# Performance work log

Hardware: AMD Instinct MI355X
Metric: run time of the kernel (lower is better)

## Reference

```python
import jax, jax.numpy as jnp
import numpy as np

D_MODEL = 1024
N_HEAD = 16
D_HEAD = D_MODEL // N_HEAD
BSZ, QLEN, MLEN = 2, 1024, 1024
KLEN = QLEN + MLEN


def setup_inputs() -> dict:
    key = jax.random.key(0)
    ks = jax.random.split(key, 10)
    s = 1.0 / np.sqrt(D_MODEL)
    inp = {
        "x": jax.random.normal(ks[0], (BSZ, QLEN, D_MODEL), jnp.float32),
        "mem": jax.random.normal(ks[1], (BSZ, MLEN, D_MODEL), jnp.float32),
        "pos_emb": jax.random.normal(ks[2], (KLEN, D_MODEL), jnp.float32),
        # causal mask with memory: query i may attend to key j iff j <= i + MLEN
        "attn_mask": (jnp.arange(KLEN)[None, :] > (jnp.arange(QLEN)[:, None] + MLEN))[None, None],
        "Wq": jax.random.normal(ks[3], (D_MODEL, D_MODEL), jnp.float32) * s,
        "Wk": jax.random.normal(ks[4], (D_MODEL, D_MODEL), jnp.float32) * s,
        "Wv": jax.random.normal(ks[5], (D_MODEL, D_MODEL), jnp.float32) * s,
        "Wr": jax.random.normal(ks[6], (D_MODEL, D_MODEL), jnp.float32) * s,
        "Wo": jax.random.normal(ks[7], (D_MODEL, D_MODEL), jnp.float32) * s,
        "r_w_bias": jax.random.normal(ks[8], (N_HEAD, D_HEAD), jnp.float32) * 0.02,
        "r_r_bias": jax.random.normal(ks[9], (N_HEAD, D_HEAD), jnp.float32) * 0.02,
    }
    return inp


def _rel_shift(x):
    # x: [b, n, q, k]
    b, n, q, k = x.shape
    x_padded = jnp.pad(x, ((0, 0), (0, 0), (0, 0), (1, 0)))  # zero column at front
    x_padded = x_padded.reshape(b, n, k + 1, q)
    return x_padded[:, :, 1:].reshape(b, n, q, k)


def reference(x, mem, pos_emb, attn_mask, Wq, Wk, Wv, Wr, Wo, r_w_bias, r_r_bias):
    bsz, qlen, _ = x.shape
    k_input = jnp.concatenate([mem, x], axis=1)
    klen = k_input.shape[1]
    scale = 1.0 / np.sqrt(D_HEAD)

    # projections -> [b, n, len, d]
    q = jnp.einsum('bqe,de->bqd', x, Wq).reshape(bsz, qlen, N_HEAD, D_HEAD).transpose(0, 2, 1, 3)
    k = jnp.einsum('bke,de->bkd', k_input, Wk).reshape(bsz, klen, N_HEAD, D_HEAD).transpose(0, 2, 1, 3)
    v = jnp.einsum('bke,de->bkd', k_input, Wv).reshape(bsz, klen, N_HEAD, D_HEAD).transpose(0, 2, 1, 3)
    r = jnp.einsum('ke,de->kd', pos_emb, Wr).reshape(klen, N_HEAD, D_HEAD).transpose(1, 0, 2)  # [n,k,d]

    AC = jnp.einsum('bnqd,bnkd->bnqk', q + r_w_bias[None, :, None, :], k)
    BD = jnp.einsum('bnqd,nkd->bnqk', q + r_r_bias[None, :, None, :], r)
    BD = _rel_shift(BD)

    attn_score = (AC + BD) * scale
    attn_score = jnp.where(attn_mask, -jnp.inf, attn_score)
    attn_prob = jax.nn.softmax(attn_score, axis=-1)

    attn_vec = jnp.einsum('bnqk,bnkd->bnqd', attn_prob, v)
    attn_vec = attn_vec.transpose(0, 2, 1, 3).reshape(bsz, qlen, N_HEAD * D_HEAD)
    return jnp.einsum('bqd,ed->bqe', attn_vec, Wo)
```

## Files before the change

kernel.cpp:

```cpp
#include <hip/hip_runtime.h>


#define B_SZ 2
#define QLEN 1024
#define MLEN 1024
#define KLEN 2048
#define DMODEL 1024
#define NH 16
#define DH 64

typedef _Float16 f16;
typedef __attribute__((ext_vector_type(8))) _Float16 f16x8;
typedef __attribute__((ext_vector_type(4))) _Float16 f16x4;
typedef __attribute__((ext_vector_type(4))) float f32x4;

__device__ __forceinline__ f16 f2h(float v) { return (f16)v; }
__device__ __forceinline__ float h2f(f16 v) { return (float)v; }

__device__ __forceinline__ f32x4 mfma16(f16x8 a, f16x8 b, f32x4 c) {
  return __builtin_amdgcn_mfma_f32_16x16x32_f16(a, b, c, 0, 0, 0);
}

__global__ __launch_bounds__(256) void convert_kernel(const float* __restrict__ src,
                                                      f16* __restrict__ dst, int n4) {
  const int i = blockIdx.x * 256 + threadIdx.x;
  if (i >= n4) return;
  const float4 v = reinterpret_cast<const float4*>(src)[i];
  f16x4 o = {(f16)v.x, (f16)v.y, (f16)v.z, (f16)v.w};
  reinterpret_cast<f16x4*>(dst)[i] = o;
}

__global__ __launch_bounds__(256) void pack_weights_kernel(
    const float* __restrict__ Wq, const float* __restrict__ Wk,
    const float* __restrict__ Wv, const float* __restrict__ Wr,
    const float* __restrict__ Wo, f16* __restrict__ Wqb, f16* __restrict__ Wkb,
    f16* __restrict__ Wvb, f16* __restrict__ Wrb, f16* __restrict__ Wob) {
  const float* src;
  f16* dst;
  switch (blockIdx.y) {
    case 0: src = Wq; dst = Wqb; break;
    case 1: src = Wk; dst = Wkb; break;
    case 2: src = Wv; dst = Wvb; break;
    case 3: src = Wr; dst = Wrb; break;
    default: src = Wo; dst = Wob; break;
  }
  const int i = blockIdx.x * 256 + threadIdx.x;
  const float4 v = reinterpret_cast<const float4*>(src)[i];
  f16x4 o = {(f16)v.x, (f16)v.y, (f16)v.z, (f16)v.w};
  reinterpret_cast<f16x4*>(dst)[i] = o;
}

__global__ __launch_bounds__(256) void build_kin_kernel(const float* __restrict__ x,
                                                        const float* __restrict__ mem,
                                                        f16* __restrict__ kin,
                                                        f16* __restrict__ xb) {
  const int i = blockIdx.x * 256 + threadIdx.x;
  const int per_b = KLEN * DMODEL / 4;
  const int b = i / per_b;
  const int rem = i - b * per_b;
  const int row = rem / (DMODEL / 4);
  const int cc = (rem - row * (DMODEL / 4)) * 4;
  const float* src = (row < MLEN)
      ? mem + ((size_t)b * MLEN + row) * DMODEL + cc
      : x + ((size_t)b * QLEN + (row - MLEN)) * DMODEL + cc;
  const float4 v = *reinterpret_cast<const float4*>(src);
  f16x4 o = {(f16)v.x, (f16)v.y, (f16)v.z, (f16)v.w};
  *reinterpret_cast<f16x4*>(kin + (size_t)i * 4) = o;
  if (row >= MLEN)
    *reinterpret_cast<f16x4*>(&xb[((size_t)b * QLEN + (row - MLEN)) * DMODEL + cc]) = o;
}

__global__ __launch_bounds__(256) void proj_kernel(
    const f16* __restrict__ Xb, const f16* __restrict__ Kin,
    const f16* __restrict__ Pos, const f16* __restrict__ Wqb,
    const f16* __restrict__ Wkb, const f16* __restrict__ Wvb,
    const f16* __restrict__ Wrb, f16* __restrict__ Qwb, f16* __restrict__ Qrb,
    f16* __restrict__ Kbb, f16* __restrict__ Vbb, f16* __restrict__ Rbb,
    const float* __restrict__ rwb, const float* __restrict__ rrb) {
  const int y = blockIdx.y;
  const f16 *A, *Bm;
  f16 *C0, *C1 = nullptr;
  int bm;
  bool dual = false;
  if (y < 16)      { A = Xb;  Bm = Wqb; C0 = Qwb; C1 = Qrb; bm = y * 128; dual = true; }
  else if (y < 48) { A = Kin; Bm = Wkb; C0 = Kbb; bm = (y - 16) * 128; }
  else if (y < 80) { A = Kin; Bm = Wvb; C0 = Vbb; bm = (y - 48) * 128; }
  else             { A = Pos; Bm = Wrb; C0 = Rbb; bm = (y - 80) * 128; }

  const int bn = blockIdx.x * 128;
  const int tid = threadIdx.x;
  const int wave = tid >> 6, lane = tid & 63;
  const int wr = wave >> 1, wc = wave & 1;
  const int lr = lane & 15, hi = lane >> 4;

  __shared__ f16 As[128][40];
  __shared__ f16 Bs[128][40];

  f32x4 acc[4][4];
#pragma unroll
  for (int m = 0; m < 4; ++m)
#pragma unroll
    for (int n = 0; n < 4; ++n) acc[m][n] = f32x4{0.f, 0.f, 0.f, 0.f};

  for (int k0 = 0; k0 < DMODEL; k0 += 32) {
#pragma unroll
    for (int it = 0; it < 2; ++it) {
      const int c = it * 256 + tid;
      const int row = c >> 2, col8 = (c & 3) << 3;
      *reinterpret_cast<f16x8*>(&As[row][col8]) =
          *reinterpret_cast<const f16x8*>(&A[(size_t)(bm + row) * DMODEL + k0 + col8]);
      *reinterpret_cast<f16x8*>(&Bs[row][col8]) =
          *reinterpret_cast<const f16x8*>(&Bm[(size_t)(bn + row) * DMODEL + k0 + col8]);
    }
    __syncthreads();
    f16x8 af[4], bf[4];
#pragma unroll
    for (int m = 0; m < 4; ++m)
      af[m] = *reinterpret_cast<const f16x8*>(&As[wr * 64 + m * 16 + lr][hi * 8]);
#pragma unroll
    for (int n = 0; n < 4; ++n)
      bf[n] = *reinterpret_cast<const f16x8*>(&Bs[wc * 64 + n * 16 + lr][hi * 8]);
#pragma unroll
    for (int m = 0; m < 4; ++m)
#pragma unroll
      for (int n = 0; n < 4; ++n) acc[m][n] = mfma16(af[m], bf[n], acc[m][n]);
    __syncthreads();
  }

#pragma unroll
  for (int m = 0; m < 4; ++m)
#pragma unroll
    for (int n = 0; n < 4; ++n)
#pragma unroll
      for (int r = 0; r < 4; ++r) {
        const int grow = bm + wr * 64 + m * 16 + hi * 4 + r;
        const int gcol = bn + wc * 64 + n * 16 + lr;
        const float v = acc[m][n][r];
        if (dual) {
          C0[(size_t)grow * DMODEL + gcol] = f2h(v + rwb[gcol]);
          C1[(size_t)grow * DMODEL + gcol] = f2h(v + rrb[gcol]);
        } else {
          C0[(size_t)grow * DMODEL + gcol] = f2h(v);
        }
      }
}

__global__ __launch_bounds__(256) void gemm_out_kernel(const f16* __restrict__ A,
                                                       const f16* __restrict__ Bm,
                                                       float* __restrict__ C) {
  const int bm = blockIdx.y * 128, bn = blockIdx.x * 128;
  const int tid = threadIdx.x;
  const int wave = tid >> 6, lane = tid & 63;
  const int wr = wave >> 1, wc = wave & 1;
  const int lr = lane & 15, hi = lane >> 4;

  __shared__ f16 As[128][40];
  __shared__ f16 Bs[128][40];

  f32x4 acc[4][4];
#pragma unroll
  for (int m = 0; m < 4; ++m)
#pragma unroll
    for (int n = 0; n < 4; ++n) acc[m][n] = f32x4{0.f, 0.f, 0.f, 0.f};

  for (int k0 = 0; k0 < DMODEL; k0 += 32) {
#pragma unroll
    for (int it = 0; it < 2; ++it) {
      const int c = it * 256 + tid;
      const int row = c >> 2, col8 = (c & 3) << 3;
      *reinterpret_cast<f16x8*>(&As[row][col8]) =
          *reinterpret_cast<const f16x8*>(&A[(size_t)(bm + row) * DMODEL + k0 + col8]);
      *reinterpret_cast<f16x8*>(&Bs[row][col8]) =
          *reinterpret_cast<const f16x8*>(&Bm[(size_t)(bn + row) * DMODEL + k0 + col8]);
    }
    __syncthreads();
    f16x8 af[4], bf[4];
#pragma unroll
    for (int m = 0; m < 4; ++m)
      af[m] = *reinterpret_cast<const f16x8*>(&As[wr * 64 + m * 16 + lr][hi * 8]);
#pragma unroll
    for (int n = 0; n < 4; ++n)
      bf[n] = *reinterpret_cast<const f16x8*>(&Bs[wc * 64 + n * 16 + lr][hi * 8]);
#pragma unroll
    for (int m = 0; m < 4; ++m)
#pragma unroll
      for (int n = 0; n < 4; ++n) acc[m][n] = mfma16(af[m], bf[n], acc[m][n]);
    __syncthreads();
  }

#pragma unroll
  for (int m = 0; m < 4; ++m)
#pragma unroll
    for (int n = 0; n < 4; ++n)
#pragma unroll
      for (int r = 0; r < 4; ++r)
        C[(size_t)(bm + wr * 64 + m * 16 + hi * 4 + r) * DMODEL + bn + wc * 64 +
          n * 16 + lr] = acc[m][n][r];
}

__global__ __launch_bounds__(512) void attn_kernel(
    const f16* __restrict__ Qw, const f16* __restrict__ Qr,
    const f16* __restrict__ Kb, const f16* __restrict__ Vb,
    const f16* __restrict__ Rb, f16* __restrict__ AV) {
  const int qb = blockIdx.x * 128;
  const int n = blockIdx.y;
  const int b = blockIdx.z;
  const int tid = threadIdx.x;
  const int wave = tid >> 6, lane = tid & 63;
  const int lr = lane & 15, hi = lane >> 4;
  const int w0 = qb + wave * 16;

  __shared__ f16 Ks[64][72];
  __shared__ f16 Vs[64][72];
  __shared__ f16 PB[8][16][72];

  f16x8 qw[2], qr[2];
  {
    const size_t qbase = ((size_t)(b * QLEN + w0 + lr)) * DMODEL + n * DH;
#pragma unroll
    for (int kk = 0; kk < 2; ++kk) {
      qw[kk] = *reinterpret_cast<const f16x8*>(&Qw[qbase + kk * 32 + hi * 8]);
      qr[kk] = *reinterpret_cast<const f16x8*>(&Qr[qbase + kk * 32 + hi * 8]);
    }
  }

  f32x4 o[4];
#pragma unroll
  for (int df = 0; df < 4; ++df) o[df] = f32x4{0.f, 0.f, 0.f, 0.f};
  float mrow[4], lrow[4];
#pragma unroll
  for (int r = 0; r < 4; ++r) { mrow[r] = -1e30f; lrow[r] = 0.f; }

  const f16* Rn = Rb + n * DH;
  const int jtiles = (qb + 128 + MLEN) >> 6;

  for (int jt = 0; jt < jtiles; ++jt) {
    const int j0 = jt << 6;
    const size_t kvbase = ((size_t)(b * KLEN + j0)) * DMODEL + n * DH;
    {
      const int c = tid;
      const int krow = c >> 3, kcol8 = (c & 7) << 3;
      *reinterpret_cast<f16x8*>(&Ks[krow][kcol8]) =
          *reinterpret_cast<const f16x8*>(&Kb[kvbase + (size_t)krow * DMODEL + kcol8]);
      const int vrow = c & 63, vcol8 = ((c >> 6) & 7) << 3;
      const f16x8 vv =
          *reinterpret_cast<const f16x8*>(&Vb[kvbase + (size_t)vrow * DMODEL + vcol8]);
#pragma unroll
      for (int e = 0; e < 8; ++e) Vs[vcol8 + e][vrow] = vv[e];
    }
    __syncthreads();

    f32x4 s[4];
#pragma unroll
    for (int nf = 0; nf < 4; ++nf) s[nf] = f32x4{0.f, 0.f, 0.f, 0.f};
#pragma unroll
    for (int kk = 0; kk < 2; ++kk)
#pragma unroll
      for (int nf = 0; nf < 4; ++nf) {
        const f16x8 kf =
            *reinterpret_cast<const f16x8*>(&Ks[nf * 16 + lr][kk * 32 + hi * 8]);
        s[nf] = mfma16(qw[kk], kf, s[nf]);
      }

    const int u0 = j0 + QLEN - 16 - w0;
    f32x4 bd[5];
#pragma unroll
    for (int nt = 0; nt < 5; ++nt) bd[nt] = f32x4{0.f, 0.f, 0.f, 0.f};
#pragma unroll
    for (int nt = 0; nt < 5; ++nt) {
      const int u = u0 + nt * 16 + lr;
      const int uc = u < KLEN ? u : KLEN - 1;
#pragma unroll
      for (int kk = 0; kk < 2; ++kk) {
        const f16x8 rf = *reinterpret_cast<const f16x8*>(
            &Rn[(size_t)uc * DMODEL + kk * 32 + hi * 8]);
        bd[nt] = mfma16(qr[kk], rf, bd[nt]);
      }
    }

    const int t0 = hi * 4;
#pragma unroll
    for (int nt = 0; nt < 5; ++nt)
#pragma unroll
      for (int r = 0; r < 4; ++r) {
        const int jl = nt * 16 + lr - 15 + t0 + r;
        if (jl >= 0 && jl < 64) PB[wave][t0 + r][jl] = f2h(bd[nt][r]);
      }
    __syncthreads();

    float sv[4][4];
#pragma unroll
    for (int r = 0; r < 4; ++r) {
      const int i = w0 + t0 + r;
#pragma unroll
      for (int nf = 0; nf < 4; ++nf) {
        const int j = j0 + nf * 16 + lr;
        sv[nf][r] = (j <= i + MLEN)
                        ? (s[nf][r] + h2f(PB[wave][t0 + r][nf * 16 + lr])) * 0.125f
                        : -1e30f;
      }
    }

#pragma unroll
    for (int r = 0; r < 4; ++r) {
      float tmax = fmaxf(fmaxf(sv[0][r], sv[1][r]), fmaxf(sv[2][r], sv[3][r]));
#pragma unroll
      for (int d = 1; d < 16; d <<= 1) tmax = fmaxf(tmax, __shfl_xor(tmax, d, 64));
      const float mnew = fmaxf(mrow[r], tmax);
      const float alpha = __expf(mrow[r] - mnew);
      mrow[r] = mnew;
      float tsum = 0.f;
#pragma unroll
      for (int nf = 0; nf < 4; ++nf) {
        const float p = __expf(sv[nf][r] - mnew);
        sv[nf][r] = p;
        tsum += p;
      }
#pragma unroll
      for (int d = 1; d < 16; d <<= 1) tsum += __shfl_xor(tsum, d, 64);
      lrow[r] = lrow[r] * alpha + tsum;
#pragma unroll
      for (int df = 0; df < 4; ++df) o[df][r] *= alpha;
    }

#pragma unroll
    for (int nf = 0; nf < 4; ++nf)
#pragma unroll
      for (int r = 0; r < 4; ++r) PB[wave][t0 + r][nf * 16 + lr] = f2h(sv[nf][r]);

#pragma unroll
    for (int kk = 0; kk < 2; ++kk) {
      const f16x8 pa =
          *reinterpret_cast<const f16x8*>(&PB[wave][lr][kk * 32 + hi * 8]);
#pragma unroll
      for (int df = 0; df < 4; ++df) {
        const f16x8 vb =
            *reinterpret_cast<const f16x8*>(&Vs[df * 16 + lr][kk * 32 + hi * 8]);
        o[df] = mfma16(pa, vb, o[df]);
      }
    }
    __syncthreads();
  }

#pragma unroll
  for (int df = 0; df < 4; ++df)
#pragma unroll
    for (int r = 0; r < 4; ++r) {
      const int i = w0 + hi * 4 + r;
      AV[((size_t)(b * QLEN + i)) * DMODEL + n * DH + df * 16 + lr] =
          f2h(o[df][r] / lrow[r]);
    }
}

extern "C" void kernel_launch(void* const* d_in, const int* in_sizes, int n_in,
                              void* d_out, int out_size, void* d_ws, size_t ws_size,
                              hipStream_t stream) {
  (void)in_sizes; (void)n_in; (void)out_size; (void)ws_size;
  const float* x   = (const float*)d_in[0];
  const float* mem = (const float*)d_in[1];
  const float* pos = (const float*)d_in[2];
  const float* Wq  = (const float*)d_in[4];
  const float* Wk  = (const float*)d_in[5];
  const float* Wv  = (const float*)d_in[6];
  const float* Wr  = (const float*)d_in[7];
  const float* Wo  = (const float*)d_in[8];
  const float* rwb = (const float*)d_in[9];
  const float* rrb = (const float*)d_in[10];
  float* out = (float*)d_out;

  char* ws = (char*)d_ws;
  size_t off = 0;
  auto alloc = [&](size_t elems) {
    void* p = (void*)(ws + off);
    off += (elems * sizeof(f16) + 255) & ~(size_t)255;
    return (f16*)p;
  };
  f16* Xb  = alloc((size_t)B_SZ * QLEN * DMODEL);
  f16* Kin = alloc((size_t)B_SZ * KLEN * DMODEL);
  f16* Pos = alloc((size_t)KLEN * DMODEL);
  f16* Wqb = alloc((size_t)DMODEL * DMODEL);
  f16* Wkb = alloc((size_t)DMODEL * DMODEL);
  f16* Wvb = alloc((size_t)DMODEL * DMODEL);
  f16* Wrb = alloc((size_t)DMODEL * DMODEL);
  f16* Wob = alloc((size_t)DMODEL * DMODEL);
  f16* Qwb = alloc((size_t)B_SZ * QLEN * DMODEL);
  f16* Qrb = alloc((size_t)B_SZ * QLEN * DMODEL);
  f16* Kbb = alloc((size_t)B_SZ * KLEN * DMODEL);
  f16* Vbb = alloc((size_t)B_SZ * KLEN * DMODEL);
  f16* Rbb = alloc((size_t)KLEN * DMODEL);
  f16* AVb = alloc((size_t)B_SZ * QLEN * DMODEL);

  pack_weights_kernel<<<dim3(1024, 5), dim3(256), 0, stream>>>(
      Wq, Wk, Wv, Wr, Wo, Wqb, Wkb, Wvb, Wrb, Wob);
  convert_kernel<<<dim3(KLEN * DMODEL / 4 / 256), dim3(256), 0, stream>>>(
      pos, Pos, KLEN * DMODEL / 4);
  build_kin_kernel<<<dim3(B_SZ * KLEN * DMODEL / 4 / 256), dim3(256), 0, stream>>>(
      x, mem, Kin, Xb);

  proj_kernel<<<dim3(8, 96), dim3(256), 0, stream>>>(
      Xb, Kin, Pos, Wqb, Wkb, Wvb, Wrb, Qwb, Qrb, Kbb, Vbb, Rbb, rwb, rrb);

  attn_kernel<<<dim3(QLEN / 128, NH, B_SZ), dim3(512), 0, stream>>>(
      Qwb, Qrb, Kbb, Vbb, Rbb, AVb);

  gemm_out_kernel<<<dim3(DMODEL / 128, B_SZ * QLEN / 128), dim3(256), 0, stream>>>(
      AVb, Wob, out);
}
```

Measured before the change: 350.1 us.

## Split attention over keys, prefetch K/V, shuffle rel-shift, direct-to-LDS GEMM loads

The GEMMs now share one core that loads 64-wide K slices straight into an XOR-swizzled LDS layout with global_load_lds, halving the barrier count per K step and avoiding bank conflicts. Attention splits each query block's key range into two halves, doubling the grid, and adds a combine kernel that merges the partial outputs using the saved row max and sum. Attention also prefetches the next K/V tile into registers while computing the current one. The relative shift is done with ds_bpermute lane shuffles instead of a round trip through LDS. The costs are an extra fp32 partial-output buffer, one more kernel launch, and higher register pressure.

After: 281.2 us. 1.25x faster.

```diff
diff --git a/kernel.cpp b/kernel.cpp
--- a/kernel.cpp
+++ b/kernel.cpp
@@ -19,6 +19,17 @@
 
 __device__ __forceinline__ f32x4 mfma16(f16x8 a, f16x8 b, f32x4 c) {
   return __builtin_amdgcn_mfma_f32_16x16x32_f16(a, b, c, 0, 0, 0);
+}
+
+__device__ __forceinline__ void gload_lds16(const f16* g, f16* l) {
+  __builtin_amdgcn_global_load_lds(
+      (const __attribute__((address_space(1))) void*)g,
+      (__attribute__((address_space(3))) void*)l, 16, 0, 0);
+}
+
+__device__ __forceinline__ float bperm(int srclane, float v) {
+  return __int_as_float(
+      __builtin_amdgcn_ds_bpermute(srclane << 2, __float_as_int(v)));
 }
 
 __global__ __launch_bounds__(256) void convert_kernel(const float* __restrict__ src,
@@ -70,6 +81,83 @@
     *reinterpret_cast<f16x4*>(&xb[((size_t)b * QLEN + (row - MLEN)) * DMODEL + cc]) = o;
 }
 
+template <int DUAL, int OUT_F32>
+__device__ __forceinline__ void gemm_core(const f16* __restrict__ A,
+                                          const f16* __restrict__ Bm,
+                                          void* __restrict__ C0v,
+                                          void* __restrict__ C1v,
+                                          const float* __restrict__ bias0,
+                                          const float* __restrict__ bias1, int bm,
+                                          int bn) {
+  const int tid = threadIdx.x;
+  const int wave = tid >> 6, lane = tid & 63;
+  const int wr = wave >> 1, wc = wave & 1;
+  const int lr = lane & 15, hi = lane >> 4;
+
+  __shared__ f16 As[128 * 64];
+  __shared__ f16 Bs[128 * 64];
+
+  f32x4 acc[4][4];
+#pragma unroll
+  for (int m = 0; m < 4; ++m)
+#pragma unroll
+    for (int n = 0; n < 4; ++n) acc[m][n] = f32x4{0.f, 0.f, 0.f, 0.f};
+
+  for (int k0 = 0; k0 < DMODEL; k0 += 64) {
+    __syncthreads();
+#pragma unroll
+    for (int it = 0; it < 4; ++it) {
+      const int c = it * 256 + tid;
+      const int row = c >> 3, c16 = c & 7;
+      const int c16s = c16 ^ (row & 7);
+      gload_lds16(&A[(size_t)(bm + row) * DMODEL + k0 + c16s * 8], &As[c * 8]);
+      gload_lds16(&Bm[(size_t)(bn + row) * DMODEL + k0 + c16s * 8], &Bs[c * 8]);
+    }
+    __syncthreads();
+#pragma unroll
+    for (int kk = 0; kk < 2; ++kk) {
+      f16x8 af[4], bf[4];
+#pragma unroll
+      for (int m = 0; m < 4; ++m) {
+        const int row = wr * 64 + m * 16 + lr;
+        const int colf = (kk * 32 + hi * 8) ^ ((row & 7) << 3);
+        af[m] = *reinterpret_cast<const f16x8*>(&As[row * 64 + colf]);
+      }
+#pragma unroll
+      for (int n = 0; n < 4; ++n) {
+        const int row = wc * 64 + n * 16 + lr;
+        const int colf = (kk * 32 + hi * 8) ^ ((row & 7) << 3);
+        bf[n] = *reinterpret_cast<const f16x8*>(&Bs[row * 64 + colf]);
+      }
+#pragma unroll
+      for (int m = 0; m < 4; ++m)
+#pragma unroll
+        for (int n = 0; n < 4; ++n) acc[m][n] = mfma16(af[m], bf[n], acc[m][n]);
+    }
+  }
+
+#pragma unroll
+  for (int m = 0; m < 4; ++m)
+#pragma unroll
+    for (int n = 0; n < 4; ++n)
+#pragma unroll
+      for (int r = 0; r < 4; ++r) {
+        const int grow = bm + wr * 64 + m * 16 + hi * 4 + r;
+        const int gcol = bn + wc * 64 + n * 16 + lr;
+        const float v = acc[m][n][r];
+        if constexpr (OUT_F32) {
+          reinterpret_cast<float*>(C0v)[(size_t)grow * DMODEL + gcol] = v;
+        } else if constexpr (DUAL) {
+          reinterpret_cast<f16*>(C0v)[(size_t)grow * DMODEL + gcol] =
+              f2h(v + bias0[gcol]);
+          reinterpret_cast<f16*>(C1v)[(size_t)grow * DMODEL + gcol] =
+              f2h(v + bias1[gcol]);
+        } else {
+          reinterpret_cast<f16*>(C0v)[(size_t)grow * DMODEL + gcol] = f2h(v);
+        }
+      }
+}
+
 __global__ __launch_bounds__(256) void proj_kernel(
     const f16* __restrict__ Xb, const f16* __restrict__ Kin,
     const f16* __restrict__ Pos, const f16* __restrict__ Wqb,
@@ -78,141 +166,47 @@
     f16* __restrict__ Kbb, f16* __restrict__ Vbb, f16* __restrict__ Rbb,
     const float* __restrict__ rwb, const float* __restrict__ rrb) {
   const int y = blockIdx.y;
-  const f16 *A, *Bm;
-  f16 *C0, *C1 = nullptr;
-  int bm;
-  bool dual = false;
-  if (y < 16)      { A = Xb;  Bm = Wqb; C0 = Qwb; C1 = Qrb; bm = y * 128; dual = true; }
-  else if (y < 48) { A = Kin; Bm = Wkb; C0 = Kbb; bm = (y - 16) * 128; }
-  else if (y < 80) { A = Kin; Bm = Wvb; C0 = Vbb; bm = (y - 48) * 128; }
-  else             { A = Pos; Bm = Wrb; C0 = Rbb; bm = (y - 80) * 128; }
-
   const int bn = blockIdx.x * 128;
-  const int tid = threadIdx.x;
-  const int wave = tid >> 6, lane = tid & 63;
-  const int wr = wave >> 1, wc = wave & 1;
-  const int lr = lane & 15, hi = lane >> 4;
-
-  __shared__ f16 As[128][40];
-  __shared__ f16 Bs[128][40];
-
-  f32x4 acc[4][4];
-#pragma unroll
-  for (int m = 0; m < 4; ++m)
-#pragma unroll
-    for (int n = 0; n < 4; ++n) acc[m][n] = f32x4{0.f, 0.f, 0.f, 0.f};
-
-  for (int k0 = 0; k0 < DMODEL; k0 += 32) {
-#pragma unroll
-    for (int it = 0; it < 2; ++it) {
-      const int c = it * 256 + tid;
-      const int row = c >> 2, col8 = (c & 3) << 3;
-      *reinterpret_cast<f16x8*>(&As[row][col8]) =
-          *reinterpret_cast<const f16x8*>(&A[(size_t)(bm + row) * DMODEL + k0 + col8]);
-      *reinterpret_cast<f16x8*>(&Bs[row][col8]) =
-          *reinterpret_cast<const f16x8*>(&Bm[(size_t)(bn + row) * DMODEL + k0 + col8]);
-    }
-    __syncthreads();
-    f16x8 af[4], bf[4];
-#pragma unroll
-    for (int m = 0; m < 4; ++m)
-      af[m] = *reinterpret_cast<const f16x8*>(&As[wr * 64 + m * 16 + lr][hi * 8]);
-#pragma unroll
-    for (int n = 0; n < 4; ++n)
-      bf[n] = *reinterpret_cast<const f16x8*>(&Bs[wc * 64 + n * 16 + lr][hi * 8]);
-#pragma unroll
-    for (int m = 0; m < 4; ++m)
-#pragma unroll
-      for (int n = 0; n < 4; ++n) acc[m][n] = mfma16(af[m], bf[n], acc[m][n]);
-    __syncthreads();
-  }
-
-#pragma unroll
-  for (int m = 0; m < 4; ++m)
-#pragma unroll
-    for (int n = 0; n < 4; ++n)
-#pragma unroll
-      for (int r = 0; r < 4; ++r) {
-        const int grow = bm + wr * 64 + m * 16 + hi * 4 + r;
-        const int gcol = bn + wc * 64 + n * 16 + lr;
-        const float v = acc[m][n][r];
-        if (dual) {
-          C0[(size_t)grow * DMODEL + gcol] = f2h(v + rwb[gcol]);
-          C1[(size_t)grow * DMODEL + gcol] = f2h(v + rrb[gcol]);
-        } else {
-          C0[(size_t)grow * DMODEL + gcol] = f2h(v);
-        }
-      }
+  if (y < 16) {
+    gemm_core<1, 0>(Xb, Wqb, Qwb, Qrb, rwb, rrb, y * 128, bn);
+  } else if (y < 48) {
+    gemm_core<0, 0>(Kin, Wkb, Kbb, nullptr, nullptr, nullptr, (y - 16) * 128, bn);
+  } else if (y < 80) {
+    gemm_core<0, 0>(Kin, Wvb, Vbb, nullptr, nullptr, nullptr, (y - 48) * 128, bn);
+  } else {
+    gemm_core<0, 0>(Pos, Wrb, Rbb, nullptr, nullptr, nullptr, (y - 80) * 128, bn);
+  }
 }
 
 __global__ __launch_bounds__(256) void gemm_out_kernel(const f16* __restrict__ A,
                                                        const f16* __restrict__ Bm,
                                                        float* __restrict__ C) {
-  const int bm = blockIdx.y * 128, bn = blockIdx.x * 128;
-  const int tid = threadIdx.x;
-  const int wave = tid >> 6, lane = tid & 63;
-  const int wr = wave >> 1, wc = wave & 1;
-  const int lr = lane & 15, hi = lane >> 4;
-
-  __shared__ f16 As[128][40];
-  __shared__ f16 Bs[128][40];
-
-  f32x4 acc[4][4];
-#pragma unroll
-  for (int m = 0; m < 4; ++m)
-#pragma unroll
-    for (int n = 0; n < 4; ++n) acc[m][n] = f32x4{0.f, 0.f, 0.f, 0.f};
-
-  for (int k0 = 0; k0 < DMODEL; k0 += 32) {
-#pragma unroll
-    for (int it = 0; it < 2; ++it) {
-      const int c = it * 256 + tid;
-      const int row = c >> 2, col8 = (c & 3) << 3;
-      *reinterpret_cast<f16x8*>(&As[row][col8]) =
-          *reinterpret_cast<const f16x8*>(&A[(size_t)(bm + row) * DMODEL + k0 + col8]);
-      *reinterpret_cast<f16x8*>(&Bs[row][col8]) =
-          *reinterpret_cast<const f16x8*>(&Bm[(size_t)(bn + row) * DMODEL + k0 + col8]);
-    }
-    __syncthreads();
-    f16x8 af[4], bf[4];
-#pragma unroll
-    for (int m = 0; m < 4; ++m)
-      af[m] = *reinterpret_cast<const f16x8*>(&As[wr * 64 + m * 16 + lr][hi * 8]);
-#pragma unroll
-    for (int n = 0; n < 4; ++n)
-      bf[n] = *reinterpret_cast<const f16x8*>(&Bs[wc * 64 + n * 16 + lr][hi * 8]);
-#pragma unroll
-    for (int m = 0; m < 4; ++m)
-#pragma unroll
-      for (int n = 0; n < 4; ++n) acc[m][n] = mfma16(af[m], bf[n], acc[m][n]);
-    __syncthreads();
-  }
-
-#pragma unroll
-  for (int m = 0; m < 4; ++m)
-#pragma unroll
-    for (int n = 0; n < 4; ++n)
-#pragma unroll
-      for (int r = 0; r < 4; ++r)
-        C[(size_t)(bm + wr * 64 + m * 16 + hi * 4 + r) * DMODEL + bn + wc * 64 +
-          n * 16 + lr] = acc[m][n][r];
+  gemm_core<0, 1>(A, Bm, C, nullptr, nullptr, nullptr, blockIdx.y * 128,
+                  blockIdx.x * 128);
 }
 
 __global__ __launch_bounds__(512) void attn_kernel(
     const f16* __restrict__ Qw, const f16* __restrict__ Qr,
     const f16* __restrict__ Kb, const f16* __restrict__ Vb,
-    const f16* __restrict__ Rb, f16* __restrict__ AV) {
-  const int qb = blockIdx.x * 128;
+    const f16* __restrict__ Rb, float* __restrict__ Opart,
+    float2* __restrict__ MLp) {
+  const int qi = blockIdx.x >> 1, half = blockIdx.x & 1;
+  const int qb = qi * 128;
   const int n = blockIdx.y;
   const int b = blockIdx.z;
   const int tid = threadIdx.x;
   const int wave = tid >> 6, lane = tid & 63;
   const int lr = lane & 15, hi = lane >> 4;
+  const int t0 = hi * 4;
   const int w0 = qb + wave * 16;
+
+  const int T = (qb + 128 + MLEN) >> 6;
+  const int jt_beg = half ? (T >> 1) : 0;
+  const int jt_end = half ? T : (T >> 1);
 
   __shared__ f16 Ks[64][72];
   __shared__ f16 Vs[64][72];
-  __shared__ f16 PB[8][16][72];
+  __shared__ f16 Ps[8][16][72];
 
   f16x8 qw[2], qr[2];
   {
@@ -232,23 +226,30 @@
   for (int r = 0; r < 4; ++r) { mrow[r] = -1e30f; lrow[r] = 0.f; }
 
   const f16* Rn = Rb + n * DH;
-  const int jtiles = (qb + 128 + MLEN) >> 6;
-
-  for (int jt = 0; jt < jtiles; ++jt) {
+
+  const int krow = tid >> 3, kc8 = (tid & 7) << 3;
+  const int vrow = tid & 63, vc8 = ((tid >> 6) & 7) << 3;
+  f16x8 kreg, vreg;
+  auto issue = [&](int jt) {
+    const size_t kvb = ((size_t)(b * KLEN + (jt << 6))) * DMODEL + n * DH;
+    kreg = *reinterpret_cast<const f16x8*>(&Kb[kvb + (size_t)krow * DMODEL + kc8]);
+    vreg = *reinterpret_cast<const f16x8*>(&Vb[kvb + (size_t)vrow * DMODEL + vc8]);
+  };
+  auto commit = [&]() {
+    *reinterpret_cast<f16x8*>(&Ks[krow][kc8]) = kreg;
+#pragma unroll
+    for (int e = 0; e < 8; ++e) Vs[vc8 + e][vrow] = vreg[e];
+  };
+
+  issue(jt_beg);
+  commit();
+  __syncthreads();
+
+  for (int jt = jt_beg; jt < jt_end; ++jt) {
+    const bool hn = (jt + 1 < jt_end);
+    if (hn) issue(jt + 1);
+
     const int j0 = jt << 6;
-    const size_t kvbase = ((size_t)(b * KLEN + j0)) * DMODEL + n * DH;
-    {
-      const int c = tid;
-      const int krow = c >> 3, kcol8 = (c & 7) << 3;
-      *reinterpret_cast<f16x8*>(&Ks[krow][kcol8]) =
-          *reinterpret_cast<const f16x8*>(&Kb[kvbase + (size_t)krow * DMODEL + kcol8]);
-      const int vrow = c & 63, vcol8 = ((c >> 6) & 7) << 3;
-      const f16x8 vv =
-          *reinterpret_cast<const f16x8*>(&Vb[kvbase + (size_t)vrow * DMODEL + vcol8]);
-#pragma unroll
-      for (int e = 0; e < 8; ++e) Vs[vcol8 + e][vrow] = vv[e];
-    }
-    __syncthreads();
 
     f32x4 s[4];
 #pragma unroll
@@ -278,32 +279,26 @@
       }
     }
 
-    const int t0 = hi * 4;
-#pragma unroll
-    for (int nt = 0; nt < 5; ++nt)
-#pragma unroll
-      for (int r = 0; r < 4; ++r) {
-        const int jl = nt * 16 + lr - 15 + t0 + r;
-        if (jl >= 0 && jl < 64) PB[wave][t0 + r][jl] = f2h(bd[nt][r]);
-      }
-    __syncthreads();
-
-    float sv[4][4];
 #pragma unroll
     for (int r = 0; r < 4; ++r) {
+      const int off = 15 - t0 - r;
+      const int sl = lr + off;
+      const int srclane = hi * 16 + (sl & 15);
+      const bool cross = sl >= 16;
       const int i = w0 + t0 + r;
 #pragma unroll
       for (int nf = 0; nf < 4; ++nf) {
+        const float x0 = bperm(srclane, bd[nf][r]);
+        const float x1 = bperm(srclane, bd[nf + 1][r]);
+        const float bv = cross ? x1 : x0;
         const int j = j0 + nf * 16 + lr;
-        sv[nf][r] = (j <= i + MLEN)
-                        ? (s[nf][r] + h2f(PB[wave][t0 + r][nf * 16 + lr])) * 0.125f
-                        : -1e30f;
+        s[nf][r] = (j <= i + MLEN) ? (s[nf][r] + bv) * 0.125f : -1e30f;
       }
     }
 
 #pragma unroll
     for (int r = 0; r < 4; ++r) {
-      float tmax = fmaxf(fmaxf(sv[0][r], sv[1][r]), fmaxf(sv[2][r], sv[3][r]));
+      float tmax = fmaxf(fmaxf(s[0][r], s[1][r]), fmaxf(s[2][r], s[3][r]));
 #pragma unroll
       for (int d = 1; d < 16; d <<= 1) tmax = fmaxf(tmax, __shfl_xor(tmax, d, 64));
       const float mnew = fmaxf(mrow[r], tmax);
@@ -312,8 +307,8 @@
       float tsum = 0.f;
 #pragma unroll
       for (int nf = 0; nf < 4; ++nf) {
-        const float p = __expf(sv[nf][r] - mnew);
-        sv[nf][r] = p;
+        const float p = __expf(s[nf][r] - mnew);
+        s[nf][r] = p;
         tsum += p;
       }
 #pragma unroll
@@ -326,12 +321,12 @@
 #pragma unroll
     for (int nf = 0; nf < 4; ++nf)
 #pragma unroll
-      for (int r = 0; r < 4; ++r) PB[wave][t0 + r][nf * 16 + lr] = f2h(sv[nf][r]);
+      for (int r = 0; r < 4; ++r) Ps[wave][t0 + r][nf * 16 + lr] = f2h(s[nf][r]);
 
 #pragma unroll
     for (int kk = 0; kk < 2; ++kk) {
       const f16x8 pa =
-          *reinterpret_cast<const f16x8*>(&PB[wave][lr][kk * 32 + hi * 8]);
+          *reinterpret_cast<const f16x8*>(&Ps[wave][lr][kk * 32 + hi * 8]);
 #pragma unroll
       for (int df = 0; df < 4; ++df) {
         const f16x8 vb =
@@ -339,17 +334,49 @@
         o[df] = mfma16(pa, vb, o[df]);
       }
     }
+
     __syncthreads();
-  }
-
+    if (hn) commit();
+    __syncthreads();
+  }
+
+  const size_t obase =
+      (((size_t)(half * B_SZ + b) * NH + n) * QLEN + w0 + t0) * DH;
 #pragma unroll
   for (int df = 0; df < 4; ++df)
 #pragma unroll
-    for (int r = 0; r < 4; ++r) {
-      const int i = w0 + hi * 4 + r;
-      AV[((size_t)(b * QLEN + i)) * DMODEL + n * DH + df * 16 + lr] =
-          f2h(o[df][r] / lrow[r]);
-    }
+    for (int r = 0; r < 4; ++r)
+      Opart[obase + (size_t)r * DH + df * 16 + lr] = o[df][r];
+  if (lr == 0) {
+    const size_t mbase = ((size_t)(half * B_SZ + b) * NH + n) * QLEN + w0 + t0;
+#pragma unroll
+    for (int r = 0; r < 4; ++r) MLp[mbase + r] = float2{mrow[r], lrow[r]};
+  }
+}
+
+__global__ __launch_bounds__(256) void combine_kernel(const float* __restrict__ Op,
+                                                      const float2* __restrict__ ML,
+                                                      f16* __restrict__ AV) {
+  const int idx = blockIdx.x * 256 + threadIdx.x;
+  const int d4 = idx & 15;
+  const int i = (idx >> 4) & 1023;
+  const int n = (idx >> 14) & 15;
+  const int b = idx >> 18;
+  const size_t r0 = ((size_t)(b * NH + n)) * QLEN + i;
+  const size_t r1 = ((size_t)((B_SZ + b) * NH + n)) * QLEN + i;
+  const float2 ml0 = ML[r0], ml1 = ML[r1];
+  const float M = fmaxf(ml0.x, ml1.x);
+  const float e0 = __expf(ml0.x - M), e1 = __expf(ml1.x - M);
+  const float inv = 1.f / (ml0.y * e0 + ml1.y * e1);
+  const float4 o0 = *reinterpret_cast<const float4*>(&Op[r0 * DH + d4 * 4]);
+  const float4 o1 = *reinterpret_cast<const float4*>(&Op[r1 * DH + d4 * 4]);
+  f16x4 out;
+  out[0] = f2h((o0.x * e0 + o1.x * e1) * inv);
+  out[1] = f2h((o0.y * e0 + o1.y * e1) * inv);
+  out[2] = f2h((o0.z * e0 + o1.z * e1) * inv);
+  out[3] = f2h((o0.w * e0 + o1.w * e1) * inv);
+  *reinterpret_cast<f16x4*>(&AV[((size_t)(b * QLEN + i)) * DMODEL + n * DH + d4 * 4]) =
+      out;
 }
 
 extern "C" void kernel_launch(void* const* d_in, const int* in_sizes, int n_in,
@@ -370,25 +397,27 @@
 
   char* ws = (char*)d_ws;
   size_t off = 0;
-  auto alloc = [&](size_t elems) {
+  auto alloc = [&](size_t bytes) {
     void* p = (void*)(ws + off);
-    off += (elems * sizeof(f16) + 255) & ~(size_t)255;
-    return (f16*)p;
+    off += (bytes + 255) & ~(size_t)255;
+    return p;
   };
-  f16* Xb  = alloc((size_t)B_SZ * QLEN * DMODEL);
-  f16* Kin = alloc((size_t)B_SZ * KLEN * DMODEL);
-  f16* Pos = alloc((size_t)KLEN * DMODEL);
-  f16* Wqb = alloc((size_t)DMODEL * DMODEL);
-  f16* Wkb = alloc((size_t)DMODEL * DMODEL);
-  f16* Wvb = alloc((size_t)DMODEL * DMODEL);
-  f16* Wrb = alloc((size_t)DMODEL * DMODEL);
-  f16* Wob = alloc((size_t)DMODEL * DMODEL);
-  f16* Qwb = alloc((size_t)B_SZ * QLEN * DMODEL);
-  f16* Qrb = alloc((size_t)B_SZ * QLEN * DMODEL);
-  f16* Kbb = alloc((size_t)B_SZ * KLEN * DMODEL);
-  f16* Vbb = alloc((size_t)B_SZ * KLEN * DMODEL);
-  f16* Rbb = alloc((size_t)KLEN * DMODEL);
-  f16* AVb = alloc((size_t)B_SZ * QLEN * DMODEL);
+  f16* Xb  = (f16*)alloc((size_t)B_SZ * QLEN * DMODEL * 2);
+  f16* Kin = (f16*)alloc((size_t)B_SZ * KLEN * DMODEL * 2);
+  f16* Pos = (f16*)alloc((size_t)KLEN * DMODEL * 2);
+  f16* Wqb = (f16*)alloc((size_t)DMODEL * DMODEL * 2);
+  f16* Wkb = (f16*)alloc((size_t)DMODEL * DMODEL * 2);
+  f16* Wvb = (f16*)alloc((size_t)DMODEL * DMODEL * 2);
+  f16* Wrb = (f16*)alloc((size_t)DMODEL * DMODEL * 2);
+  f16* Wob = (f16*)alloc((size_t)DMODEL * DMODEL * 2);
+  f16* Qwb = (f16*)alloc((size_t)B_SZ * QLEN * DMODEL * 2);
+  f16* Qrb = (f16*)alloc((size_t)B_SZ * QLEN * DMODEL * 2);
+  f16* Kbb = (f16*)alloc((size_t)B_SZ * KLEN * DMODEL * 2);
+  f16* Vbb = (f16*)alloc((size_t)B_SZ * KLEN * DMODEL * 2);
+  f16* Rbb = (f16*)alloc((size_t)KLEN * DMODEL * 2);
+  f16* AVb = (f16*)alloc((size_t)B_SZ * QLEN * DMODEL * 2);
+  float*  Opart = (float*)alloc((size_t)2 * B_SZ * NH * QLEN * DH * 4);
+  float2* MLp   = (float2*)alloc((size_t)2 * B_SZ * NH * QLEN * 8);
 
   pack_weights_kernel<<<dim3(1024, 5), dim3(256), 0, stream>>>(
       Wq, Wk, Wv, Wr, Wo, Wqb, Wkb, Wvb, Wrb, Wob);
@@ -400,8 +429,11 @@
   proj_kernel<<<dim3(8, 96), dim3(256), 0, stream>>>(
       Xb, Kin, Pos, Wqb, Wkb, Wvb, Wrb, Qwb, Qrb, Kbb, Vbb, Rbb, rwb, rrb);
 
-  attn_kernel<<<dim3(QLEN / 128, NH, B_SZ), dim3(512), 0, stream>>>(
-      Qwb, Qrb, Kbb, Vbb, Rbb, AVb);
+  attn_kernel<<<dim3(QLEN / 128 * 2, NH, B_SZ), dim3(512), 0, stream>>>(
+      Qwb, Qrb, Kbb, Vbb, Rbb, Opart, MLp);
+
+  combine_kernel<<<dim3(B_SZ * NH * QLEN * (DH / 4) / 256), dim3(256), 0, stream>>>(
+      Opart, MLp, AVb);
 
   gemm_out_kernel<<<dim3(DMODEL / 128, B_SZ * QLEN / 128), dim3(256), 0, stream>>>(
       AVb, Wob, out);
```
